# Kernel optimization log

Measured on AMD Instinct MI355X. Metric: run time of the kernel, lower is better.

The kernel has to match this reference:

```python
import jax, jax.numpy as jnp
import numpy as np

# --- static config (matches init_kwargs) ---
DEPTH, HEADS, DIM, EMBED, TXT_DIM = 4, 16, 1024, 768, 4096
T, GH, GW, N_TEXT = 8, 14, 14, 16          # temporal blocks, grid H, grid W, text tokens
HD = DIM // HEADS                          # head dim = 64
SCALE = HD ** -0.5
MLP_H = int(4.0 * DIM)
F_TOK = T * GH * GW                        # frame tokens = 1568


def _ln(x, w, b, eps=1e-5):
    m = jnp.mean(x, axis=-1, keepdims=True)
    v = jnp.var(x, axis=-1, keepdims=True)
    return (x - m) * jax.lax.rsqrt(v + eps) * w + b


def _rope_cos_sin():
    # 3D axial RoPE over (frame, height, width); per-axis rotary dim d=2*((HD//3)//2)=20.
    d = 2 * ((HD // 3) // 2)
    ids = jnp.arange(F_TOK)
    hw = GH * GW
    pos = jnp.stack([ids // hw, (ids % hw) // GW, ids % GW], 0).astype(jnp.float32)  # [3,F]
    omega = jnp.arange(d // 2, dtype=jnp.float32) / (d / 2.0)
    inv = 1.0 / (10000.0 ** omega)                       # [d/2]
    freq = pos[:, :, None] * inv                          # [3,F,d/2]
    freq = jnp.repeat(freq, 2, axis=-1)                   # interleaved pairs -> [3,F,d]
    freq = jnp.concatenate([freq[0], freq[1], freq[2]], -1)  # [F, 3d]
    freq = jnp.pad(freq, ((0, 0), (0, HD - 3 * d)))       # remainder dims: identity rotation
    freq = jnp.pad(freq, ((N_TEXT, 0), (0, 0)))           # text tokens: identity rotation
    return jnp.cos(freq), jnp.sin(freq)                   # each [N, HD]


def _rot_pairs(x):
    # (x0,x1) -> (-x1,x0) on interleaved pairs
    x2 = x.reshape(x.shape[:-1] + (HD // 2, 2))
    return jnp.stack([-x2[..., 1], x2[..., 0]], -1).reshape(x.shape)


def _mask_bias():
    # text-text: causal tril; frame->text: full; frame-frame: block-causal by frame id
    N = N_TEXT + F_TOK
    m = np.zeros((N, N), dtype=bool)
    m[:N_TEXT, :N_TEXT] = np.tril(np.ones((N_TEXT, N_TEXT), dtype=bool))
    m[N_TEXT:, :N_TEXT] = True
    fid = np.arange(F_TOK) // (GH * GW)
    m[N_TEXT:, N_TEXT:] = fid[None, :] <= fid[:, None]
    return jnp.where(jnp.asarray(m), 0.0, -1e9).astype(jnp.float32)


def _block(x, p, cos, sin, bias):
    (ln1_w, ln1_b, qkv_w, qkv_b, proj_w, proj_b,
     ln2_w, ln2_b, fc1_w, fc1_b, fc2_w, fc2_b) = p
    B, N, _ = x.shape
    h = _ln(x, ln1_w, ln1_b)
    qkv = (h @ qkv_w + qkv_b).reshape(B, N, 3, HEADS, HD).transpose(2, 0, 3, 1, 4)
    q, k, v = qkv[0], qkv[1], qkv[2]                      # [B,H,N,HD]
    q = q * cos + _rot_pairs(q) * sin
    k = k * cos + _rot_pairs(k) * sin
    att = jnp.einsum("bhqd,bhkd->bhqk", q, k) * SCALE + bias
    att = jax.nn.softmax(att, axis=-1)
    o = jnp.einsum("bhqk,bhkd->bhqd", att, v).transpose(0, 2, 1, 3).reshape(B, N, DIM)
    x = x + o @ proj_w + proj_b
    h = _ln(x, ln2_w, ln2_b)
    h = jax.nn.gelu(h @ fc1_w + fc1_b, approximate=False)
    return x + h @ fc2_w + fc2_b


def setup_inputs() -> dict:
    key = jax.random.key(0)
    ks = jax.random.split(key, 10)
    std = 0.02
    W = lambda k, s: jax.random.normal(k, s, jnp.float32) * std
    inp = {
        "x": jax.random.normal(ks[0], (1, F_TOK, EMBED), jnp.float32),
        "text_instruction": jax.random.normal(ks[1], (1, N_TEXT, TXT_DIM), jnp.float32),
        "w_embed": W(ks[2], (EMBED, DIM)), "b_embed": jnp.zeros((DIM,), jnp.float32),
        "w_text": W(ks[3], (TXT_DIM, DIM)), "b_text": jnp.zeros((DIM,), jnp.float32),
        "ln1_w": jnp.ones((DEPTH, DIM), jnp.float32), "ln1_b": jnp.zeros((DEPTH, DIM), jnp.float32),
        "qkv_w": W(ks[4], (DEPTH, DIM, 3 * DIM)), "qkv_b": jnp.zeros((DEPTH, 3 * DIM), jnp.float32),
        "proj_w": W(ks[5], (DEPTH, DIM, DIM)), "proj_b": jnp.zeros((DEPTH, DIM), jnp.float32),
        "ln2_w": jnp.ones((DEPTH, DIM), jnp.float32), "ln2_b": jnp.zeros((DEPTH, DIM), jnp.float32),
        "fc1_w": W(ks[6], (DEPTH, DIM, MLP_H)), "fc1_b": jnp.zeros((DEPTH, MLP_H), jnp.float32),
        "fc2_w": W(ks[7], (DEPTH, MLP_H, DIM)), "fc2_b": jnp.zeros((DEPTH, DIM), jnp.float32),
        "normf_w": jnp.ones((DIM,), jnp.float32), "normf_b": jnp.zeros((DIM,), jnp.float32),
        "w_out": W(ks[8], (DIM, EMBED)), "b_out": jnp.zeros((EMBED,), jnp.float32),
    }
    # _rescale_blocks: proj and fc2 weights divided by sqrt(2*layer_id)
    sc = 1.0 / jnp.sqrt(2.0 * (jnp.arange(DEPTH, dtype=jnp.float32) + 1.0))
    inp["proj_w"] = inp["proj_w"] * sc[:, None, None]
    inp["fc2_w"] = inp["fc2_w"] * sc[:, None, None]
    return inp


def reference(x, text_instruction, w_embed, b_embed, w_text, b_text,
              ln1_w, ln1_b, qkv_w, qkv_b, proj_w, proj_b,
              ln2_w, ln2_b, fc1_w, fc1_b, fc2_w, fc2_b,
              normf_w, normf_b, w_out, b_out):
    h = x @ w_embed + b_embed                      # predictor_embed
    t = text_instruction @ w_text + b_text         # text_encoder
    h = jnp.concatenate([t, h], axis=1)            # [B, N_TEXT + F_TOK, DIM]
    cos, sin = _rope_cos_sin()
    bias = _mask_bias()
    params = (ln1_w, ln1_b, qkv_w, qkv_b, proj_w, proj_b,
              ln2_w, ln2_b, fc1_w, fc1_b, fc2_w, fc2_b)
    def step(carry, p):
        return _block(carry, p, cos, sin, bias), None
    h, _ = jax.lax.scan(step, h, params)
    h = h[:, N_TEXT:, :]                           # drop text tokens
    h = _ln(h, normf_w, normf_b)
    return h @ w_out + b_out                       # predictor_proj -> [B, F_TOK, EMBED]
```

## Files before the change

### kernel.cpp

```cpp
#include <hip/hip_runtime.h>
#include <hip/hip_bf16.h>
#include <math.h>

#define HEADS 16
#define DIM 1024
#define N_TEXT 16
#define F_TOK 1568
#define NTOK 1584
#define MPAD 1664
#define SCALEF 0.125f

typedef unsigned int uint;
typedef unsigned short u16;

typedef __bf16 bf16x8 __attribute__((ext_vector_type(8)));
typedef float f32x4 __attribute__((ext_vector_type(4)));

__device__ inline u16 f2b(float f){
  uint u = __builtin_bit_cast(uint, f);
  uint r = u + 0x7fffu + ((u >> 16) & 1u);
  return (u16)(r >> 16);
}

__device__ inline f32x4 mfma16(bf16x8 a, bf16x8 b, f32x4 c){
  return __builtin_amdgcn_mfma_f32_16x16x32_bf16(a, b, c, 0, 0, 0);
}

__device__ __forceinline__ void gload16(const u16* g, u16* l){
  __builtin_amdgcn_global_load_lds(
      (__attribute__((address_space(1))) u16*)const_cast<u16*>(g),
      (__attribute__((address_space(3))) u16*)l, 16, 0, 0);
}

__global__ __launch_bounds__(256) void wtrans_kernel(const float* __restrict__ src,
                                                     u16* __restrict__ dst, int K, int N){
  __shared__ float tile[32][33];
  int n0 = blockIdx.x * 32, k0 = blockIdx.y * 32;
  int t = threadIdx.x;
  int col = t & 31, rb = t >> 5;
#pragma unroll
  for (int p = 0; p < 4; ++p){
    int row = p*8 + rb;
    tile[row][col] = src[(size_t)(k0+row)*N + n0 + col];
  }
  __syncthreads();
#pragma unroll
  for (int p = 0; p < 4; ++p){
    int rn = p*8 + rb;
    dst[(size_t)(n0+rn)*K + k0 + col] = f2b(tile[col][rn]);
  }
}

__global__ __launch_bounds__(256) void f2b_kernel(const float* __restrict__ src,
                                                  u16* __restrict__ dst, int n){
  int i = blockIdx.x*256 + threadIdx.x;
  if (i < n) dst[i] = f2b(src[i]);
}

__global__ __launch_bounds__(256) void rope_table_kernel(float* __restrict__ ct,
                                                         float* __restrict__ st){
  int i = blockIdx.x*256 + threadIdx.x;
  if (i >= NTOK*64) return;
  int n = i >> 6, d = i & 63;
  float f = 0.f;
  if (n >= N_TEXT){
    int id = n - N_TEXT;
    int p0 = id / 196;
    int p1 = (id % 196) / 14;
    int p2 = id % 14;
    float pos = 0.f; int j = -1;
    if (d < 20){ pos = (float)p0; j = d >> 1; }
    else if (d < 40){ pos = (float)p1; j = (d-20) >> 1; }
    else if (d < 60){ pos = (float)p2; j = (d-40) >> 1; }
    if (j >= 0){
      float inv = powf(10000.f, -(float)j * 0.1f);
      f = pos * inv;
    }
  }
  ct[i] = cosf(f);
  st[i] = sinf(f);
}

__global__ __launch_bounds__(256) void rope_apply_kernel(const float* __restrict__ qkv,
    const float* __restrict__ ct, const float* __restrict__ st,
    u16* __restrict__ qb, u16* __restrict__ kb, u16* __restrict__ vb){
  int i = blockIdx.x*256 + threadIdx.x;
  if (i >= NTOK*HEADS*32) return;
  int n = i / 512;
  int rem = i & 511;
  int h = rem >> 5;
  int d0 = (rem & 31) * 2;
  size_t base = (size_t)n*3072 + h*64 + d0;
  float q0 = qkv[base],      q1 = qkv[base+1];
  float k0 = qkv[base+1024], k1 = qkv[base+1025];
  float v0 = qkv[base+2048], v1 = qkv[base+2049];
  float c = ct[n*64+d0], s = st[n*64+d0];
  size_t ob = ((size_t)h*MPAD + n)*64 + d0;
  qb[ob]   = f2b(q0*c - q1*s);
  qb[ob+1] = f2b(q1*c + q0*s);
  kb[ob]   = f2b(k0*c - k1*s);
  kb[ob+1] = f2b(k1*c + k0*s);
  vb[ob]   = f2b(v0);
  vb[ob+1] = f2b(v1);
}

__global__ __launch_bounds__(256) void ln_kernel(const float* __restrict__ x,
    const float* __restrict__ w, const float* __restrict__ b, u16* __restrict__ out){
  int row = blockIdx.x, t = threadIdx.x;
  const float* xr = x + (size_t)row * DIM;
  float4 v = *(const float4*)&xr[t*4];
  float s = v.x+v.y+v.z+v.w;
  float ss = v.x*v.x+v.y*v.y+v.z*v.z+v.w*v.w;
#pragma unroll
  for (int o=32;o>0;o>>=1){ s += __shfl_down(s,o,64); ss += __shfl_down(ss,o,64); }
  __shared__ float red[8];
  int wid = t>>6;
  if ((t&63)==0){ red[wid] = s; red[4+wid] = ss; }
  __syncthreads();
  float S = red[0]+red[1]+red[2]+red[3];
  float SS = red[4]+red[5]+red[6]+red[7];
  float mean = S * (1.0f/1024.0f);
  float var = SS * (1.0f/1024.0f) - mean*mean;
  float inv = rsqrtf(var + 1e-5f);
  ushort4 o4;
  o4.x = f2b((v.x-mean)*inv*w[t*4+0]+b[t*4+0]);
  o4.y = f2b((v.y-mean)*inv*w[t*4+1]+b[t*4+1]);
  o4.z = f2b((v.z-mean)*inv*w[t*4+2]+b[t*4+2]);
  o4.w = f2b((v.w-mean)*inv*w[t*4+3]+b[t*4+3]);
  *(ushort4*)&out[(size_t)row*DIM + t*4] = o4;
}

template<int EPI>
__global__ __launch_bounds__(256, 2)
void gemm2_kernel(const u16* __restrict__ A, const u16* __restrict__ BT,
                  const float* __restrict__ bias,
                  float* __restrict__ outF, u16* __restrict__ outB,
                  int M, int N, int K, int klen, size_t partStride)
{
  __shared__ u16 L[2][2][128*64];
  const int t = threadIdx.x, wid = t >> 6, lane = t & 63;
  const int lr = lane & 15, lg = lane >> 4;
  const int wr = wid >> 1, wc = wid & 1;
  const int m0 = blockIdx.y * 128, n0 = blockIdx.x * 128;
  const int kstart = blockIdx.z * klen;

  const int srow = lane >> 3;
  const int scol = ((lane & 7) ^ srow) * 8;
  const u16* Ast = A  + (size_t)(m0 + srow)*K + kstart + scol;
  const u16* Bst = BT + (size_t)(n0 + srow)*K + kstart + scol;

  const int s0 = (lg     ) ^ (lr & 7);
  const int s1 = (lg + 4 ) ^ (lr & 7);
  const int aBase = (wr*64 + lr)*64;
  const int bBase = (wc*64 + lr)*64;

  f32x4 acc[4][4] = {};
  const int nk = klen >> 6;

  auto STAGE = [&](int buf, int step){
    const u16* a = Ast + (size_t)step*64;
    const u16* b = Bst + (size_t)step*64;
#pragma unroll
    for (int j = 0; j < 4; ++j){
      int c = wid*4 + j;
      gload16(a + (size_t)c*8*K, &L[buf][0][c*512]);
      gload16(b + (size_t)c*8*K, &L[buf][1][c*512]);
    }
  };

  STAGE(0, 0);
  __syncthreads();
  int cur = 0;
  for (int tt = 0; tt < nk; ++tt){
    if (tt + 1 < nk) STAGE(cur ^ 1, tt + 1);
    const u16* Ab = &L[cur][0][0];
    const u16* Bb = &L[cur][1][0];
    bf16x8 af[2][4], bv[2][4];
#pragma unroll
    for (int m = 0; m < 4; ++m){
      af[0][m] = *(const bf16x8*)&Ab[aBase + m*1024 + s0*8];
      af[1][m] = *(const bf16x8*)&Ab[aBase + m*1024 + s1*8];
    }
#pragma unroll
    for (int n = 0; n < 4; ++n){
      bv[0][n] = *(const bf16x8*)&Bb[bBase + n*1024 + s0*8];
      bv[1][n] = *(const bf16x8*)&Bb[bBase + n*1024 + s1*8];
    }
#pragma unroll
    for (int ks = 0; ks < 2; ++ks)
#pragma unroll
      for (int m = 0; m < 4; ++m)
#pragma unroll
        for (int n = 0; n < 4; ++n)
          acc[m][n] = mfma16(af[ks][m], bv[ks][n], acc[m][n]);
    __syncthreads();
    cur ^= 1;
  }

#pragma unroll
  for (int m = 0; m < 4; ++m){
#pragma unroll
    for (int r = 0; r < 4; ++r){
      int row = m0 + wr*64 + m*16 + lg*4 + r;
      if (row >= M) continue;
#pragma unroll
      for (int n = 0; n < 4; ++n){
        int col = n0 + wc*64 + n*16 + lr;
        float v = acc[m][n][r];
        if constexpr (EPI == 4){
          outF[partStride*blockIdx.z + (size_t)row*N + col] = v;
        } else if constexpr (EPI == 3){
          v += bias[col];
          v = 0.5f * v * (1.0f + erff(v * 0.70710678118654752f));
          outB[(size_t)row*N + col] = f2b(v);
        } else {
          v += bias[col];
          outF[(size_t)row*N + col] = v;
        }
      }
    }
  }
}

__global__ __launch_bounds__(256) void reduce_kernel(const float* __restrict__ part,
    size_t stride, int S, const float* __restrict__ bias, const float* __restrict__ resid,
    float* __restrict__ out, int MN, int N){
  int i = (blockIdx.x*256 + threadIdx.x)*4;
  if (i >= MN) return;
  float4 v = *(const float4*)&bias[i % N];
  if (resid){
    float4 r = *(const float4*)&resid[i];
    v.x += r.x; v.y += r.y; v.z += r.z; v.w += r.w;
  }
  for (int s = 0; s < S; ++s){
    float4 p = *(const float4*)&part[(size_t)s*stride + i];
    v.x += p.x; v.y += p.y; v.z += p.z; v.w += p.w;
  }
  *(float4*)&out[i] = v;
}

__global__ __launch_bounds__(256)
void attn_kernel(const u16* __restrict__ qb, const u16* __restrict__ kb,
                 const u16* __restrict__ vb, u16* __restrict__ ob)
{
  __shared__ u16 Kl[64][72];
  __shared__ u16 Vl[64][72];
  __shared__ u16 Pl[64][72];
  const int hh = blockIdx.y;
  const int q0 = blockIdx.x * 64;
  const int t = threadIdx.x, wid = t>>6, lane = t&63, lr = lane&15, lg = lane>>4;
  const size_t hbase = (size_t)hh*MPAD*64;

  bf16x8 qf[2];
  {
    int row = q0 + wid*16 + lr;
    qf[0] = *(const bf16x8*)&qb[hbase + (size_t)row*64 + lg*8];
    qf[1] = *(const bf16x8*)&qb[hbase + (size_t)row*64 + 32 + lg*8];
  }

  int lim[4];
#pragma unroll
  for (int r=0;r<4;++r){
    int qi = q0 + wid*16 + lg*4 + r;
    int L = (qi < N_TEXT) ? (qi + 1) : (16 + ((qi - 16)/196 + 1)*196);
    lim[r] = min(L, NTOK);
  }
  const int qlast = min(q0 + 63, NTOK - 1);
  const int kend  = (qlast < N_TEXT) ? (qlast + 1)
                                     : min(16 + ((qlast - 16)/196 + 1)*196, NTOK);
  const int nkt = (kend + 63) >> 6;

  float mrun[4], lrun[4];
#pragma unroll
  for (int i=0;i<4;++i){ mrun[i] = -3.0e38f; lrun[i] = 0.0f; }
  f32x4 oacc[4] = {};

  for (int kbi = 0; kbi < nkt; ++kbi){
    const int k0 = kbi*64;
#pragma unroll
    for (int p=0;p<2;++p){
      int sidx = t + p*256;
      int row = sidx >> 3, c8 = (sidx & 7) * 8;
      *(uint4*)&Kl[row][c8] = *(const uint4*)&kb[hbase + (size_t)(k0 + row)*64 + c8];
    }
#pragma unroll
    for (int p=0;p<2;++p){
      int sidx = t + p*256;
      int kk = sidx & 63, d8 = (sidx >> 6) * 8;
      union { uint4 u; u16 s[8]; } tv;
      tv.u = *(const uint4*)&vb[hbase + (size_t)(k0 + kk)*64 + d8];
#pragma unroll
      for (int j=0;j<8;++j) Vl[d8+j][kk] = tv.s[j];
    }
    __syncthreads();

    f32x4 sacc[4] = {};
#pragma unroll
    for (int n=0;n<4;++n){
      bf16x8 kf0 = *(const bf16x8*)&Kl[n*16 + lr][lg*8];
      bf16x8 kf1 = *(const bf16x8*)&Kl[n*16 + lr][32 + lg*8];
      sacc[n] = mfma16(qf[0], kf0, sacc[n]);
      sacc[n] = mfma16(qf[1], kf1, sacc[n]);
    }

    float sval[4][4];
    float pmax[4] = {-3.0e38f, -3.0e38f, -3.0e38f, -3.0e38f};
#pragma unroll
    for (int n=0;n<4;++n){
      int ki = k0 + n*16 + lr;
#pragma unroll
      for (int r=0;r<4;++r){
        float v = (ki < lim[r]) ? sacc[n][r]*SCALEF : -3.0e38f;
        sval[n][r] = v;
        pmax[r] = fmaxf(pmax[r], v);
      }
    }
#pragma unroll
    for (int r=0;r<4;++r){
      float v = pmax[r];
      v = fmaxf(v, __shfl_xor(v,1,64));
      v = fmaxf(v, __shfl_xor(v,2,64));
      v = fmaxf(v, __shfl_xor(v,4,64));
      v = fmaxf(v, __shfl_xor(v,8,64));
      pmax[r] = v;
    }
    float alpha[4], psum[4];
#pragma unroll
    for (int r=0;r<4;++r){
      float mnew = fmaxf(mrun[r], pmax[r]);
      alpha[r] = __expf(mrun[r] - mnew);
      mrun[r] = mnew;
      psum[r] = 0.f;
    }
#pragma unroll
    for (int r=0;r<4;++r){
      float mn = mrun[r];
#pragma unroll
      for (int n=0;n<4;++n){
        float p = __expf(sval[n][r] - mn);
        psum[r] += p;
        Pl[wid*16 + lg*4 + r][n*16 + lr] = f2b(p);
      }
    }
#pragma unroll
    for (int r=0;r<4;++r){
      float v = psum[r];
      v += __shfl_xor(v,1,64); v += __shfl_xor(v,2,64);
      v += __shfl_xor(v,4,64); v += __shfl_xor(v,8,64);
      lrun[r] = lrun[r]*alpha[r] + v;
    }
#pragma unroll
    for (int n=0;n<4;++n)
#pragma unroll
      for (int r=0;r<4;++r)
        oacc[n][r] *= alpha[r];
    __syncthreads();

    bf16x8 pf0 = *(const bf16x8*)&Pl[wid*16 + lr][lg*8];
    bf16x8 pf1 = *(const bf16x8*)&Pl[wid*16 + lr][32 + lg*8];
#pragma unroll
    for (int n=0;n<4;++n){
      bf16x8 vf0 = *(const bf16x8*)&Vl[n*16 + lr][lg*8];
      bf16x8 vf1 = *(const bf16x8*)&Vl[n*16 + lr][32 + lg*8];
      oacc[n] = mfma16(pf0, vf0, oacc[n]);
      oacc[n] = mfma16(pf1, vf1, oacc[n]);
    }
    __syncthreads();
  }

#pragma unroll
  for (int n=0;n<4;++n)
#pragma unroll
    for (int r=0;r<4;++r){
      int row = q0 + wid*16 + lg*4 + r;
      int col = hh*64 + n*16 + lr;
      ob[(size_t)row*DIM + col] = f2b(oacc[n][r] / lrun[r]);
    }
}

extern "C" void kernel_launch(void* const* d_in, const int* in_sizes, int n_in,
                              void* d_out, int out_size, void* d_ws, size_t ws_size,
                              hipStream_t stream)
{
  const float* x       = (const float*)d_in[0];
  const float* text    = (const float*)d_in[1];
  const float* w_embed = (const float*)d_in[2];
  const float* b_embed = (const float*)d_in[3];
  const float* w_text  = (const float*)d_in[4];
  const float* b_text  = (const float*)d_in[5];
  const float* ln1_w   = (const float*)d_in[6];
  const float* ln1_b   = (const float*)d_in[7];
  const float* qkv_w   = (const float*)d_in[8];
  const float* qkv_b   = (const float*)d_in[9];
  const float* proj_w  = (const float*)d_in[10];
  const float* proj_b  = (const float*)d_in[11];
  const float* ln2_w   = (const float*)d_in[12];
  const float* ln2_b   = (const float*)d_in[13];
  const float* fc1_w   = (const float*)d_in[14];
  const float* fc1_b   = (const float*)d_in[15];
  const float* fc2_w   = (const float*)d_in[16];
  const float* fc2_b   = (const float*)d_in[17];
  const float* normf_w = (const float*)d_in[18];
  const float* normf_b = (const float*)d_in[19];
  const float* w_out   = (const float*)d_in[20];
  const float* b_out   = (const float*)d_in[21];
  (void)in_sizes; (void)n_in; (void)out_size;

  char* ws = (char*)d_ws;
  size_t off = 0;
  auto alloc = [&](size_t bytes)->void*{
    void* p = ws + off; off += (bytes + 255) & ~(size_t)255; return p;
  };
  u16* wTe  = (u16*)alloc((size_t)1024*768*2);
  u16* wTt  = (u16*)alloc((size_t)1024*4096*2);
  u16* wTq  = (u16*)alloc((size_t)4*3072*1024*2);
  u16* wTp  = (u16*)alloc((size_t)4*1024*1024*2);
  u16* wT1  = (u16*)alloc((size_t)4*4096*1024*2);
  u16* wT2  = (u16*)alloc((size_t)4*1024*4096*2);
  u16* wTo  = (u16*)alloc((size_t)768*1024*2);
  u16* xbf  = (u16*)alloc((size_t)MPAD*768*2);
  u16* tbf  = (u16*)alloc((size_t)128*4096*2);
  float* h  = (float*)alloc((size_t)MPAD*1024*4);
  u16* lno  = (u16*)alloc((size_t)MPAD*1024*2);
  float* qkv= (float*)alloc((size_t)MPAD*3072*4);
  u16* qbuf = (u16*)alloc((size_t)HEADS*MPAD*64*2);
  u16* kbuf = (u16*)alloc((size_t)HEADS*MPAD*64*2);
  u16* vbuf = (u16*)alloc((size_t)HEADS*MPAD*64*2);
  u16* obf  = (u16*)alloc((size_t)MPAD*1024*2);
  u16* mlp  = (u16*)alloc((size_t)MPAD*4096*2);
  float* ct = (float*)alloc((size_t)NTOK*64*4);
  float* st = (float*)alloc((size_t)NTOK*64*4);
  float* partF = (float*)alloc((size_t)4*MPAD*1024*4);
  if (off > ws_size) return;
  float* projPart = (float*)mlp;

  wtrans_kernel<<<dim3(1024/32, 768/32), 256, 0, stream>>>(w_embed, wTe, 768, 1024);
  wtrans_kernel<<<dim3(1024/32, 4096/32), 256, 0, stream>>>(w_text, wTt, 4096, 1024);
  for (int l=0;l<4;++l){
    wtrans_kernel<<<dim3(3072/32, 1024/32),256,0,stream>>>(qkv_w + (size_t)l*1024*3072, wTq + (size_t)l*3072*1024, 1024, 3072);
    wtrans_kernel<<<dim3(1024/32, 1024/32),256,0,stream>>>(proj_w + (size_t)l*1024*1024, wTp + (size_t)l*1024*1024, 1024, 1024);
    wtrans_kernel<<<dim3(4096/32, 1024/32),256,0,stream>>>(fc1_w + (size_t)l*1024*4096, wT1 + (size_t)l*4096*1024, 1024, 4096);
    wtrans_kernel<<<dim3(1024/32, 4096/32),256,0,stream>>>(fc2_w + (size_t)l*4096*1024, wT2 + (size_t)l*1024*4096, 4096, 1024);
  }
  wtrans_kernel<<<dim3(768/32, 1024/32),256,0,stream>>>(w_out, wTo, 1024, 768);

  f2b_kernel<<<(F_TOK*768+255)/256,256,0,stream>>>(x, xbf, F_TOK*768);
  f2b_kernel<<<(16*4096+255)/256,256,0,stream>>>(text, tbf, 16*4096);
  rope_table_kernel<<<(NTOK*64+255)/256,256,0,stream>>>(ct, st);

  gemm2_kernel<4><<<dim3(8,1,8),256,0,stream>>>(tbf, wTt, nullptr, partF, nullptr,
      16, 1024, 4096, 512, (size_t)16*1024);
  reduce_kernel<<<(16*1024/4+255)/256,256,0,stream>>>(partF, (size_t)16*1024, 8, b_text, nullptr, h, 16*1024, 1024);
  gemm2_kernel<0><<<dim3(8,13,1),256,0,stream>>>(xbf, wTe, b_embed, h + (size_t)16*1024, nullptr,
      1568, 1024, 768, 768, 0);

  for (int l=0;l<4;++l){
    ln_kernel<<<MPAD,256,0,stream>>>(h, ln1_w + l*1024, ln1_b + l*1024, lno);
    gemm2_kernel<0><<<dim3(24,13,1),256,0,stream>>>(lno, wTq + (size_t)l*3072*1024, qkv_b + l*3072,
        qkv, nullptr, MPAD, 3072, 1024, 1024, 0);
    rope_apply_kernel<<<(NTOK*512+255)/256,256,0,stream>>>(qkv, ct, st, qbuf, kbuf, vbuf);
    attn_kernel<<<dim3(MPAD/64,16),256,0,stream>>>(qbuf, kbuf, vbuf, obf);
    gemm2_kernel<4><<<dim3(8,13,2),256,0,stream>>>(obf, wTp + (size_t)l*1024*1024, nullptr,
        projPart, nullptr, MPAD, 1024, 1024, 512, (size_t)MPAD*1024);
    reduce_kernel<<<(MPAD*1024/4+255)/256,256,0,stream>>>(projPart, (size_t)MPAD*1024, 2,
        proj_b + l*1024, h, h, MPAD*1024, 1024);
    ln_kernel<<<MPAD,256,0,stream>>>(h, ln2_w + l*1024, ln2_b + l*1024, lno);
    gemm2_kernel<3><<<dim3(32,13,1),256,0,stream>>>(lno, wT1 + (size_t)l*4096*1024, fc1_b + l*4096,
        nullptr, mlp, MPAD, 4096, 1024, 1024, 0);
    gemm2_kernel<4><<<dim3(8,13,4),256,0,stream>>>(mlp, wT2 + (size_t)l*1024*4096, nullptr,
        partF, nullptr, MPAD, 1024, 4096, 1024, (size_t)MPAD*1024);
    reduce_kernel<<<(MPAD*1024/4+255)/256,256,0,stream>>>(partF, (size_t)MPAD*1024, 4,
        fc2_b + l*1024, h, h, MPAD*1024, 1024);
  }

  ln_kernel<<<F_TOK,256,0,stream>>>(h + (size_t)16*1024, normf_w, normf_b, lno);
  gemm2_kernel<4><<<dim3(6,13,4),256,0,stream>>>(lno, wTo, nullptr, partF, nullptr,
      F_TOK, 768, 1024, 256, (size_t)F_TOK*768);
  reduce_kernel<<<(F_TOK*768/4+255)/256,256,0,stream>>>(partF, (size_t)F_TOK*768, 4,
      b_out, nullptr, (float*)d_out, F_TOK*768, 768);
}
```

Before: 1.067 ms.

## Split attention over key blocks with a separate log-sum-exp combine kernel

The attention kernel now splits each query tile's key range into NSPLIT chunks along a third grid dimension. Each chunk writes unnormalized fp32 partial outputs plus its running max and sum. A new combine kernel merges the chunks with log-sum-exp weighting and writes the bf16 output. The aim is to raise parallelism and even out the load from the block-causal mask, where late query tiles scan many more keys than early ones. The cost is extra fp32 partial traffic through the workspace and one more kernel launch per layer.

```diff
diff --git a/kernel.cpp b/kernel.cpp
--- a/kernel.cpp
+++ b/kernel.cpp
@@ -9,6 +9,7 @@
 #define NTOK 1584
 #define MPAD 1664
 #define SCALEF 0.125f
+#define NSPLIT 4
 
 typedef unsigned int uint;
 typedef unsigned short u16;
@@ -240,16 +241,19 @@
 }
 
 __global__ __launch_bounds__(256)
-void attn_kernel(const u16* __restrict__ qb, const u16* __restrict__ kb,
-                 const u16* __restrict__ vb, u16* __restrict__ ob)
+void attn_split_kernel(const u16* __restrict__ qb, const u16* __restrict__ kb,
+                       const u16* __restrict__ vb, float* __restrict__ attO,
+                       float* __restrict__ attM, float* __restrict__ attL)
 {
   __shared__ u16 Kl[64][72];
   __shared__ u16 Vl[64][72];
   __shared__ u16 Pl[64][72];
   const int hh = blockIdx.y;
   const int q0 = blockIdx.x * 64;
+  const int zz = blockIdx.z;
   const int t = threadIdx.x, wid = t>>6, lane = t&63, lr = lane&15, lg = lane>>4;
   const size_t hbase = (size_t)hh*MPAD*64;
+  const size_t pbase = (size_t)(zz*HEADS + hh)*MPAD;
 
   bf16x8 qf[2];
   {
@@ -269,13 +273,16 @@
   const int kend  = (qlast < N_TEXT) ? (qlast + 1)
                                      : min(16 + ((qlast - 16)/196 + 1)*196, NTOK);
   const int nkt = (kend + 63) >> 6;
+  const int tpz = (nkt + NSPLIT - 1) / NSPLIT;
+  const int kb0 = zz * tpz;
+  const int kb1 = min(nkt, kb0 + tpz);
 
   float mrun[4], lrun[4];
 #pragma unroll
   for (int i=0;i<4;++i){ mrun[i] = -3.0e38f; lrun[i] = 0.0f; }
   f32x4 oacc[4] = {};
 
-  for (int kbi = 0; kbi < nkt; ++kbi){
+  for (int kbi = kb0; kbi < kb1; ++kbi){
     const int k0 = kbi*64;
 #pragma unroll
     for (int p=0;p<2;++p){
@@ -373,9 +380,46 @@
 #pragma unroll
     for (int r=0;r<4;++r){
       int row = q0 + wid*16 + lg*4 + r;
-      int col = hh*64 + n*16 + lr;
-      ob[(size_t)row*DIM + col] = f2b(oacc[n][r] / lrun[r]);
-    }
+      attO[(pbase + row)*64 + n*16 + lr] = oacc[n][r];
+    }
+  if (lr == 0){
+#pragma unroll
+    for (int r=0;r<4;++r){
+      int row = q0 + wid*16 + lg*4 + r;
+      attM[pbase + row] = mrun[r];
+      attL[pbase + row] = lrun[r];
+    }
+  }
+}
+
+__global__ __launch_bounds__(256)
+void attn_combine_kernel(const float* __restrict__ attO, const float* __restrict__ attM,
+                         const float* __restrict__ attL, u16* __restrict__ ob)
+{
+  int i = blockIdx.x*256 + threadIdx.x;
+  if (i >= MPAD*HEADS*16) return;
+  int dchunk = i & 15;
+  int head = (i >> 4) & 15;
+  int row = i >> 8;
+  float m = -3.0e38f;
+#pragma unroll
+  for (int z=0; z<NSPLIT; ++z)
+    m = fmaxf(m, attM[(size_t)(z*HEADS+head)*MPAD + row]);
+  float l = 0.f;
+  float4 o = {0.f,0.f,0.f,0.f};
+#pragma unroll
+  for (int z=0; z<NSPLIT; ++z){
+    size_t pb = (size_t)(z*HEADS+head)*MPAD + row;
+    float w = __expf(attM[pb] - m);
+    l += w * attL[pb];
+    float4 p = *(const float4*)&attO[pb*64 + dchunk*4];
+    o.x += w*p.x; o.y += w*p.y; o.z += w*p.z; o.w += w*p.w;
+  }
+  float inv = 1.0f / fmaxf(l, 1e-30f);
+  ushort4 o4;
+  o4.x = f2b(o.x*inv); o4.y = f2b(o.y*inv);
+  o4.z = f2b(o.z*inv); o4.w = f2b(o.w*inv);
+  *(ushort4*)&ob[(size_t)row*DIM + head*64 + dchunk*4] = o4;
 }
 
 extern "C" void kernel_launch(void* const* d_in, const int* in_sizes, int n_in,
@@ -431,6 +475,8 @@
   float* ct = (float*)alloc((size_t)NTOK*64*4);
   float* st = (float*)alloc((size_t)NTOK*64*4);
   float* partF = (float*)alloc((size_t)4*MPAD*1024*4);
+  float* attM = (float*)alloc((size_t)NSPLIT*HEADS*MPAD*4);
+  float* attL = (float*)alloc((size_t)NSPLIT*HEADS*MPAD*4);
   if (off > ws_size) return;
   float* projPart = (float*)mlp;
 
@@ -459,7 +505,9 @@
     gemm2_kernel<0><<<dim3(24,13,1),256,0,stream>>>(lno, wTq + (size_t)l*3072*1024, qkv_b + l*3072,
         qkv, nullptr, MPAD, 3072, 1024, 1024, 0);
     rope_apply_kernel<<<(NTOK*512+255)/256,256,0,stream>>>(qkv, ct, st, qbuf, kbuf, vbuf);
-    attn_kernel<<<dim3(MPAD/64,16),256,0,stream>>>(qbuf, kbuf, vbuf, obf);
+    attn_split_kernel<<<dim3(MPAD/64,HEADS,NSPLIT),256,0,stream>>>(qbuf, kbuf, vbuf,
+        partF, attM, attL);
+    attn_combine_kernel<<<(MPAD*HEADS*16+255)/256,256,0,stream>>>(partF, attM, attL, obf);
     gemm2_kernel<4><<<dim3(8,13,2),256,0,stream>>>(obf, wTp + (size_t)l*1024*1024, nullptr,
         projPart, nullptr, MPAD, 1024, 1024, 512, (size_t)MPAD*1024);
     reduce_kernel<<<(MPAD*1024/4+255)/256,256,0,stream>>>(projPart, (size_t)MPAD*1024, 2,
```

Result: faster. 985.4 us (-7.6%).
